# Kernel tuning notes

Measured on AMD Instinct MI355X. Metric: run time of the kernel, lower is better.

The kernel has to match this reference:

```python
import jax, jax.numpy as jnp
import numpy as np

N_EMBD = 1024
N_HEAD = 16

def setup_inputs() -> dict:
    key = jax.random.key(0)
    ks = jax.random.split(key, 5)
    x = jax.random.normal(ks[0], (4, 2048, N_EMBD), dtype=jnp.float32)
    # torch Linear default init ~ U(-1/sqrt(fan_in), 1/sqrt(fan_in)); use scaled normals
    s = 1.0 / np.sqrt(N_EMBD)
    W_attn = jax.random.normal(ks[1], (N_EMBD, 3 * N_EMBD), dtype=jnp.float32) * s
    b_attn = jax.random.normal(ks[2], (3 * N_EMBD,), dtype=jnp.float32) * s
    W_proj = jax.random.normal(ks[3], (N_EMBD, N_EMBD), dtype=jnp.float32) * s
    b_proj = jax.random.normal(ks[4], (N_EMBD,), dtype=jnp.float32) * s
    return {"x": x, "W_attn": W_attn, "b_attn": b_attn, "W_proj": W_proj, "b_proj": b_proj}

def reference(x, W_attn, b_attn, W_proj, b_proj) -> jnp.ndarray:
    B, T, C = x.shape
    H = N_HEAD
    D = C // H  # head dim
    qkv = x @ W_attn + b_attn  # [B,T,3C]
    q, k, v = jnp.split(qkv, 3, axis=-1)
    # [B,T,C] -> [B,H,T,D]
    q = q.reshape(B, T, H, D).transpose(0, 2, 1, 3)
    k = k.reshape(B, T, H, D).transpose(0, 2, 1, 3)
    v = v.reshape(B, T, H, D).transpose(0, 2, 1, 3)
    scale = 1.0 / jnp.sqrt(jnp.float32(D))
    att = jnp.einsum('bhqd,bhkd->bhqk', q, k) * scale  # [B,H,T,T]
    causal = jnp.tril(jnp.ones((T, T), dtype=bool))
    att = jnp.where(causal[None, None, :, :], att, -jnp.inf)
    att = jax.nn.softmax(att, axis=-1)
    y = jnp.einsum('bhqk,bhkd->bhqd', att, v)  # [B,H,T,D]
    y = y.transpose(0, 2, 1, 3).reshape(B, T, C)
    return y @ W_proj + b_proj
```

## Files before the change

### kernel.cpp

```cpp
#include <hip/hip_runtime.h>
#include <stdint.h>


typedef __attribute__((ext_vector_type(8))) short short8;
typedef __attribute__((ext_vector_type(4))) float floatx4;

#define AS1C(p) ((const __attribute__((address_space(1))) void*)(p))
#define AS3(p)  ((__attribute__((address_space(3))) void*)(p))

__device__ __forceinline__ unsigned short f2bf(float f) {
  unsigned int u = __builtin_bit_cast(unsigned int, f);
  u = (u + 0x7fffu + ((u >> 16) & 1u)) >> 16;
  return (unsigned short)u;
}
__device__ __forceinline__ unsigned short f2bf_trunc(float f) {
  return (unsigned short)(__builtin_bit_cast(unsigned int, f) >> 16);
}

__global__ void k_cvt(const float* __restrict__ in, unsigned short* __restrict__ out, int n4) {
  int i = blockIdx.x * blockDim.x + threadIdx.x;
  if (i < n4) {
    float4 v = ((const float4*)in)[i];
    ushort4 o;
    o.x = f2bf(v.x); o.y = f2bf(v.y); o.z = f2bf(v.z); o.w = f2bf(v.w);
    ((ushort4*)out)[i] = o;
  }
}

__global__ void k_tw(const float* __restrict__ in, unsigned short* __restrict__ out, int K, int N) {
  __shared__ float t[32][33];
  int n0 = blockIdx.x * 32, k0 = blockIdx.y * 32;
  int tx = threadIdx.x, ty = threadIdx.y;
#pragma unroll
  for (int i = 0; i < 4; i++)
    t[ty + 8 * i][tx] = in[(size_t)(k0 + ty + 8 * i) * N + n0 + tx];
  __syncthreads();
#pragma unroll
  for (int i = 0; i < 4; i++)
    out[(size_t)(n0 + ty + 8 * i) * K + k0 + tx] = f2bf(t[tx][ty + 8 * i]);
}

__global__ void k_tv(const unsigned short* __restrict__ qkv, unsigned short* __restrict__ vt) {
  __shared__ unsigned short t[32][33];
  int t0 = blockIdx.x * 32;
  int d0 = blockIdx.y * 32;
  int bh = blockIdx.z;
  int b = bh >> 4, h = bh & 15;
  int tx = threadIdx.x, ty = threadIdx.y;
#pragma unroll
  for (int i = 0; i < 4; i++)
    t[ty + 8 * i][tx] = qkv[(size_t)(b * 2048 + t0 + ty + 8 * i) * 3072 + 2048 + h * 64 + d0 + tx];
  __syncthreads();
#pragma unroll
  for (int i = 0; i < 4; i++)
    vt[(size_t)(bh * 64 + d0 + ty + 8 * i) * 2048 + t0 + tx] = t[tx][ty + 8 * i];
}

template <int OUT_F32>
__global__ __launch_bounds__(256)
void k_gemm(const unsigned short* __restrict__ A,
            const unsigned short* __restrict__ Bt,
            const float* __restrict__ bias,
            void* __restrict__ Cout, int M, int N, int K) {
  __shared__ unsigned short lA[128 * 64];
  __shared__ unsigned short lB[128 * 64];
  int tid = threadIdx.x;
  int lane = tid & 63, wv = tid >> 6;
  int lc = lane & 15, quad = lane >> 4;
  int m0 = blockIdx.y * 128, n0 = blockIdx.x * 128;
  int wm = (wv >> 1) * 64, wn = (wv & 1) * 64;
  int sw = lc & 7;

  floatx4 acc[4][4];
#pragma unroll
  for (int i = 0; i < 4; i++)
#pragma unroll
    for (int j = 0; j < 4; j++) acc[i][j] = (floatx4){0.f, 0.f, 0.f, 0.f};

  int srow = tid >> 3;
  int scol = (((tid & 7) ^ (srow & 7))) * 8;
  const unsigned short* gA = A + (size_t)(m0 + srow) * K + scol;
  const unsigned short* gB = Bt + (size_t)(n0 + srow) * K + scol;

  for (int k0 = 0; k0 < K; k0 += 64) {
#pragma unroll
    for (int c = 0; c < 4; c++) {
      __builtin_amdgcn_global_load_lds(AS1C(gA + (size_t)(32 * c) * K + k0),
                                       AS3(lA + (32 * c + 8 * wv) * 64), 16, 0, 0);
      __builtin_amdgcn_global_load_lds(AS1C(gB + (size_t)(32 * c) * K + k0),
                                       AS3(lB + (32 * c + 8 * wv) * 64), 16, 0, 0);
    }
    __syncthreads();
#pragma unroll
    for (int s = 0; s < 2; s++) {
      short8 af[4], bfr[4];
#pragma unroll
      for (int i = 0; i < 4; i++)
        af[i] = *(const short8*)(lA + (wm + i * 16 + lc) * 64 + (((s * 4 + quad) ^ sw) * 8));
#pragma unroll
      for (int j = 0; j < 4; j++)
        bfr[j] = *(const short8*)(lB + (wn + j * 16 + lc) * 64 + (((s * 4 + quad) ^ sw) * 8));
#pragma unroll
      for (int i = 0; i < 4; i++)
#pragma unroll
        for (int j = 0; j < 4; j++)
          acc[i][j] = __builtin_amdgcn_mfma_f32_16x16x32_bf16(af[i], bfr[j], acc[i][j], 0, 0, 0);
    }
    __syncthreads();
  }

  float bv[4];
#pragma unroll
  for (int j = 0; j < 4; j++) bv[j] = bias[n0 + wn + j * 16 + lc];
#pragma unroll
  for (int i = 0; i < 4; i++) {
#pragma unroll
    for (int j = 0; j < 4; j++) {
#pragma unroll
      for (int r = 0; r < 4; r++) {
        size_t idx = (size_t)(m0 + wm + i * 16 + quad * 4 + r) * N + (n0 + wn + j * 16 + lc);
        float v = acc[i][j][r] + bv[j];
        if (OUT_F32) ((float*)Cout)[idx] = v;
        else         ((unsigned short*)Cout)[idx] = f2bf(v);
      }
    }
  }
}

#define LP_STRIDE 68
__global__ __launch_bounds__(256, 4)
void k_flash(const unsigned short* __restrict__ qkv,
             const unsigned short* __restrict__ vt,
             unsigned short* __restrict__ y) {
  __shared__ unsigned short lK[64 * 64];
  __shared__ unsigned short lVT[64 * 64];
  __shared__ unsigned short lP[4][2][16 * LP_STRIDE];
  int tid = threadIdx.x, lane = tid & 63, wv = tid >> 6;
  int lc = lane & 15, quad = lane >> 4;
  int sw = lc & 7;
  int j  = blockIdx.x;
  int bh = blockIdx.y;
  int b = bh >> 4, h = bh & 15;
  int qtA = j, qtB = 31 - j;
  int qrA = qtA * 64 + wv * 16;
  int qrB = qtB * 64 + wv * 16;

  short8 qfA[2], qfB[2];
  {
    const unsigned short* qp = qkv + (size_t)(b * 2048 + qrA + lc) * 3072 + h * 64 + quad * 8;
    qfA[0] = *(const short8*)qp;
    qfA[1] = *(const short8*)(qp + 32);
  }
  {
    const unsigned short* qp = qkv + (size_t)(b * 2048 + qrB + lc) * 3072 + h * 64 + quad * 8;
    qfB[0] = *(const short8*)qp;
    qfB[1] = *(const short8*)(qp + 32);
  }

  float rsA[4] = {0.f, 0.f, 0.f, 0.f}, rsB[4] = {0.f, 0.f, 0.f, 0.f};
  floatx4 oA[4], oB[4];
#pragma unroll
  for (int dt = 0; dt < 4; dt++) {
    oA[dt] = (floatx4){0.f, 0.f, 0.f, 0.f};
    oB[dt] = (floatx4){0.f, 0.f, 0.f, 0.f};
  }

  int srow = tid >> 3;
  int scol = ((tid & 7) ^ (srow & 7)) * 8;
  const unsigned short* gK = qkv + (size_t)(b * 2048 + srow) * 3072 + 1024 + h * 64 + scol;
  const unsigned short* gV = vt + (size_t)(bh * 64 + srow) * 2048 + scol;

  const float SC2 = 0.18033688011f;
  int nt = qtB + 1;

  for (int kv = 0; kv < nt; kv++) {
    int kv0 = kv * 64;
#pragma unroll
    for (int c = 0; c < 2; c++) {
      __builtin_amdgcn_global_load_lds(AS1C(gK + (size_t)(kv0 + 32 * c) * 3072),
                                       AS3(lK + (32 * c + 8 * wv) * 64), 16, 0, 0);
      __builtin_amdgcn_global_load_lds(AS1C(gV + (size_t)(32 * c) * 2048 + kv0),
                                       AS3(lVT + (32 * c + 8 * wv) * 64), 16, 0, 0);
    }
    __syncthreads();

    bool withA = (kv <= qtA);

    floatx4 sB[4], sA[4];
#pragma unroll
    for (int n = 0; n < 4; n++) {
      short8 kf0 = *(const short8*)(lK + (n * 16 + lc) * 64 + ((quad ^ sw) * 8));
      short8 kf1 = *(const short8*)(lK + (n * 16 + lc) * 64 + (((4 + quad) ^ sw) * 8));
      floatx4 t = (floatx4){0.f, 0.f, 0.f, 0.f};
      t = __builtin_amdgcn_mfma_f32_16x16x32_bf16(qfB[0], kf0, t, 0, 0, 0);
      t = __builtin_amdgcn_mfma_f32_16x16x32_bf16(qfB[1], kf1, t, 0, 0, 0);
      sB[n] = t;
      if (withA) {
        floatx4 u = (floatx4){0.f, 0.f, 0.f, 0.f};
        u = __builtin_amdgcn_mfma_f32_16x16x32_bf16(qfA[0], kf0, u, 0, 0, 0);
        u = __builtin_amdgcn_mfma_f32_16x16x32_bf16(qfA[1], kf1, u, 0, 0, 0);
        sA[n] = u;
      }
    }

    {
      bool diag = (kv == qtB);
#pragma unroll
      for (int n = 0; n < 4; n++)
#pragma unroll
        for (int r = 0; r < 4; r++) {
          float arg = sB[n][r] * SC2;
          if (diag && (kv0 + n * 16 + lc > qrB + quad * 4 + r)) arg = -__builtin_inff();
          float p = __builtin_amdgcn_exp2f(arg);
          rsB[r] += p;
          lP[wv][0][(quad * 4 + r) * LP_STRIDE + n * 16 + lc] = f2bf_trunc(p);
        }
    }
    if (withA) {
      bool diag = (kv == qtA);
#pragma unroll
      for (int n = 0; n < 4; n++)
#pragma unroll
        for (int r = 0; r < 4; r++) {
          float arg = sA[n][r] * SC2;
          if (diag && (kv0 + n * 16 + lc > qrA + quad * 4 + r)) arg = -__builtin_inff();
          float p = __builtin_amdgcn_exp2f(arg);
          rsA[r] += p;
          lP[wv][1][(quad * 4 + r) * LP_STRIDE + n * 16 + lc] = f2bf_trunc(p);
        }
    }

#pragma unroll
    for (int s2 = 0; s2 < 2; s2++) {
      short8 pfB = *(const short8*)(&lP[wv][0][0] + lc * LP_STRIDE + s2 * 32 + quad * 8);
      short8 pfA;
      if (withA) pfA = *(const short8*)(&lP[wv][1][0] + lc * LP_STRIDE + s2 * 32 + quad * 8);
#pragma unroll
      for (int dt = 0; dt < 4; dt++) {
        short8 vf = *(const short8*)(lVT + (dt * 16 + lc) * 64 + (((s2 * 4 + quad) ^ sw) * 8));
        oB[dt] = __builtin_amdgcn_mfma_f32_16x16x32_bf16(pfB, vf, oB[dt], 0, 0, 0);
        if (withA) oA[dt] = __builtin_amdgcn_mfma_f32_16x16x32_bf16(pfA, vf, oA[dt], 0, 0, 0);
      }
    }
    __syncthreads();
  }

#pragma unroll
  for (int off = 1; off < 16; off <<= 1)
#pragma unroll
    for (int r = 0; r < 4; r++) {
      rsA[r] += __shfl_xor(rsA[r], off);
      rsB[r] += __shfl_xor(rsB[r], off);
    }
#pragma unroll
  for (int r = 0; r < 4; r++) {
    float invA = 1.0f / rsA[r];
    float invB = 1.0f / rsB[r];
#pragma unroll
    for (int dt = 0; dt < 4; dt++) {
      size_t ia = (size_t)(b * 2048 + qrA + quad * 4 + r) * 1024 + h * 64 + dt * 16 + lc;
      size_t ib = (size_t)(b * 2048 + qrB + quad * 4 + r) * 1024 + h * 64 + dt * 16 + lc;
      y[ia] = f2bf(oA[dt][r] * invA);
      y[ib] = f2bf(oB[dt][r] * invB);
    }
  }
}

extern "C" void kernel_launch(void* const* d_in, const int* in_sizes, int n_in,
                              void* d_out, int out_size, void* d_ws, size_t ws_size,
                              hipStream_t stream) {
  const float* x      = (const float*)d_in[0];
  const float* W_attn = (const float*)d_in[1];
  const float* b_attn = (const float*)d_in[2];
  const float* W_proj = (const float*)d_in[3];
  const float* b_proj = (const float*)d_in[4];

  char* ws = (char*)d_ws;
  unsigned short* xb     = (unsigned short*)ws;
  unsigned short* wattnT = (unsigned short*)(ws + 16777216);
  unsigned short* wprojT = (unsigned short*)(ws + 23068672);
  unsigned short* qkv    = (unsigned short*)(ws + 25165824);
  unsigned short* vt     = (unsigned short*)(ws + 75497472);
  unsigned short* y      = xb;

  k_cvt<<<8192, 256, 0, stream>>>(x, xb, 8388608 / 4);
  k_tw<<<dim3(96, 32), dim3(32, 8), 0, stream>>>(W_attn, wattnT, 1024, 3072);
  k_tw<<<dim3(32, 32), dim3(32, 8), 0, stream>>>(W_proj, wprojT, 1024, 1024);
  k_gemm<0><<<dim3(24, 64), 256, 0, stream>>>(xb, wattnT, b_attn, qkv, 8192, 3072, 1024);
  k_tv<<<dim3(64, 2, 64), dim3(32, 8), 0, stream>>>(qkv, vt);
  k_flash<<<dim3(16, 64), 256, 0, stream>>>(qkv, vt, y);
  k_gemm<1><<<dim3(8, 64), 256, 0, stream>>>(y, wprojT, b_proj, d_out, 8192, 1024, 1024);
}
```

Before: 271.0 us.

## Double-buffer K tiles, fold softmax scale into QKV GEMM, share P buffer

Adds a second LDS buffer for K so the next tile's K load is issued while the current tile is computed, and waits on only part of the vector-memory counter before the PV MFMAs. Removes the per-score scale multiply by folding the softmax scale into the Q columns in the QKV GEMM epilogue. Processes the B and A query tiles sequentially through one shared per-wave P buffer to cut LDS use. The hand-coded waitcnt immediate and the reuse of one P buffer add ordering risk. Folding the scale before the bf16 rounding of Q slightly changes numerics.

Measured after the change: 286.0 us. 5.6% more time.

```diff
diff --git a/kernel.cpp b/kernel.cpp
--- a/kernel.cpp
+++ b/kernel.cpp
@@ -7,6 +7,8 @@
 
 #define AS1C(p) ((const __attribute__((address_space(1))) void*)(p))
 #define AS3(p)  ((__attribute__((address_space(3))) void*)(p))
+
+#define SC2F 0.18033688011f
 
 __device__ __forceinline__ unsigned short f2bf(float f) {
   unsigned int u = __builtin_bit_cast(unsigned int, f);
@@ -116,10 +118,11 @@
   for (int i = 0; i < 4; i++) {
 #pragma unroll
     for (int j = 0; j < 4; j++) {
+      float sc = (!OUT_F32 && (n0 + wn + j * 16) < 1024) ? SC2F : 1.0f;
 #pragma unroll
       for (int r = 0; r < 4; r++) {
         size_t idx = (size_t)(m0 + wm + i * 16 + quad * 4 + r) * N + (n0 + wn + j * 16 + lc);
-        float v = acc[i][j][r] + bv[j];
+        float v = (acc[i][j][r] + bv[j]) * sc;
         if (OUT_F32) ((float*)Cout)[idx] = v;
         else         ((unsigned short*)Cout)[idx] = f2bf(v);
       }
@@ -132,9 +135,9 @@
 void k_flash(const unsigned short* __restrict__ qkv,
              const unsigned short* __restrict__ vt,
              unsigned short* __restrict__ y) {
-  __shared__ unsigned short lK[64 * 64];
+  __shared__ unsigned short lK[2][64 * 64];
   __shared__ unsigned short lVT[64 * 64];
-  __shared__ unsigned short lP[4][2][16 * LP_STRIDE];
+  __shared__ unsigned short lP[4][16 * LP_STRIDE];
   int tid = threadIdx.x, lane = tid & 63, wv = tid >> 6;
   int lc = lane & 15, quad = lane >> 4;
   int sw = lc & 7;
@@ -170,27 +173,35 @@
   const unsigned short* gK = qkv + (size_t)(b * 2048 + srow) * 3072 + 1024 + h * 64 + scol;
   const unsigned short* gV = vt + (size_t)(bh * 64 + srow) * 2048 + scol;
 
-  const float SC2 = 0.18033688011f;
   int nt = qtB + 1;
+
+#pragma unroll
+  for (int c = 0; c < 2; c++)
+    __builtin_amdgcn_global_load_lds(AS1C(gK + (size_t)(32 * c) * 3072),
+                                     AS3(lK[0] + (32 * c + 8 * wv) * 64), 16, 0, 0);
 
   for (int kv = 0; kv < nt; kv++) {
     int kv0 = kv * 64;
-#pragma unroll
-    for (int c = 0; c < 2; c++) {
-      __builtin_amdgcn_global_load_lds(AS1C(gK + (size_t)(kv0 + 32 * c) * 3072),
-                                       AS3(lK + (32 * c + 8 * wv) * 64), 16, 0, 0);
+    __syncthreads();
+
+#pragma unroll
+    for (int c = 0; c < 2; c++)
       __builtin_amdgcn_global_load_lds(AS1C(gV + (size_t)(32 * c) * 2048 + kv0),
                                        AS3(lVT + (32 * c + 8 * wv) * 64), 16, 0, 0);
-    }
-    __syncthreads();
-
+    int kp = (kv + 1 < nt) ? kv + 1 : kv;
+#pragma unroll
+    for (int c = 0; c < 2; c++)
+      __builtin_amdgcn_global_load_lds(AS1C(gK + (size_t)(kp * 64 + 32 * c) * 3072),
+                                       AS3(lK[(kv + 1) & 1] + (32 * c + 8 * wv) * 64), 16, 0, 0);
+
+    const unsigned short* kb = lK[kv & 1];
     bool withA = (kv <= qtA);
 
     floatx4 sB[4], sA[4];
 #pragma unroll
     for (int n = 0; n < 4; n++) {
-      short8 kf0 = *(const short8*)(lK + (n * 16 + lc) * 64 + ((quad ^ sw) * 8));
-      short8 kf1 = *(const short8*)(lK + (n * 16 + lc) * 64 + (((4 + quad) ^ sw) * 8));
+      short8 kf0 = *(const short8*)(kb + (n * 16 + lc) * 64 + ((quad ^ sw) * 8));
+      short8 kf1 = *(const short8*)(kb + (n * 16 + lc) * 64 + (((4 + quad) ^ sw) * 8));
       floatx4 t = (floatx4){0.f, 0.f, 0.f, 0.f};
       t = __builtin_amdgcn_mfma_f32_16x16x32_bf16(qfB[0], kf0, t, 0, 0, 0);
       t = __builtin_amdgcn_mfma_f32_16x16x32_bf16(qfB[1], kf1, t, 0, 0, 0);
@@ -209,40 +220,48 @@
       for (int n = 0; n < 4; n++)
 #pragma unroll
         for (int r = 0; r < 4; r++) {
-          float arg = sB[n][r] * SC2;
+          float arg = sB[n][r];
           if (diag && (kv0 + n * 16 + lc > qrB + quad * 4 + r)) arg = -__builtin_inff();
           float p = __builtin_amdgcn_exp2f(arg);
           rsB[r] += p;
-          lP[wv][0][(quad * 4 + r) * LP_STRIDE + n * 16 + lc] = f2bf_trunc(p);
+          lP[wv][(quad * 4 + r) * LP_STRIDE + n * 16 + lc] = f2bf_trunc(p);
         }
     }
+
+    __builtin_amdgcn_s_waitcnt(0x0F72);
+
+#pragma unroll
+    for (int s2 = 0; s2 < 2; s2++) {
+      short8 pfB = *(const short8*)(&lP[wv][0] + lc * LP_STRIDE + s2 * 32 + quad * 8);
+#pragma unroll
+      for (int dt = 0; dt < 4; dt++) {
+        short8 vf = *(const short8*)(lVT + (dt * 16 + lc) * 64 + (((s2 * 4 + quad) ^ sw) * 8));
+        oB[dt] = __builtin_amdgcn_mfma_f32_16x16x32_bf16(pfB, vf, oB[dt], 0, 0, 0);
+      }
+    }
+
     if (withA) {
       bool diag = (kv == qtA);
 #pragma unroll
       for (int n = 0; n < 4; n++)
 #pragma unroll
         for (int r = 0; r < 4; r++) {
-          float arg = sA[n][r] * SC2;
+          float arg = sA[n][r];
           if (diag && (kv0 + n * 16 + lc > qrA + quad * 4 + r)) arg = -__builtin_inff();
           float p = __builtin_amdgcn_exp2f(arg);
           rsA[r] += p;
-          lP[wv][1][(quad * 4 + r) * LP_STRIDE + n * 16 + lc] = f2bf_trunc(p);
+          lP[wv][(quad * 4 + r) * LP_STRIDE + n * 16 + lc] = f2bf_trunc(p);
         }
-    }
-
-#pragma unroll
-    for (int s2 = 0; s2 < 2; s2++) {
-      short8 pfB = *(const short8*)(&lP[wv][0][0] + lc * LP_STRIDE + s2 * 32 + quad * 8);
-      short8 pfA;
-      if (withA) pfA = *(const short8*)(&lP[wv][1][0] + lc * LP_STRIDE + s2 * 32 + quad * 8);
-#pragma unroll
-      for (int dt = 0; dt < 4; dt++) {
-        short8 vf = *(const short8*)(lVT + (dt * 16 + lc) * 64 + (((s2 * 4 + quad) ^ sw) * 8));
-        oB[dt] = __builtin_amdgcn_mfma_f32_16x16x32_bf16(pfB, vf, oB[dt], 0, 0, 0);
-        if (withA) oA[dt] = __builtin_amdgcn_mfma_f32_16x16x32_bf16(pfA, vf, oA[dt], 0, 0, 0);
+#pragma unroll
+      for (int s2 = 0; s2 < 2; s2++) {
+        short8 pfA = *(const short8*)(&lP[wv][0] + lc * LP_STRIDE + s2 * 32 + quad * 8);
+#pragma unroll
+        for (int dt = 0; dt < 4; dt++) {
+          short8 vf = *(const short8*)(lVT + (dt * 16 + lc) * 64 + (((s2 * 4 + quad) ^ sw) * 8));
+          oA[dt] = __builtin_amdgcn_mfma_f32_16x16x32_bf16(pfA, vf, oA[dt], 0, 0, 0);
+        }
       }
     }
-    __syncthreads();
   }
 
 #pragma unroll
```

## Remap blocks for XCD-local L2 reuse and fold softmax scale into Q

Applied to the files above, without the earlier changes.

Both GEMMs and the flash-attention kernel now launch a 1D grid and remap the block index so consecutive blocks on the same XCD share row tiles or the same batch-head. This is meant to improve L2 locality on the multi-XCD MI355X. Separately, the attention scale (log2e/sqrt(D)) is applied to the Q columns in the QKV GEMM epilogue, which removes a multiply per score in the flash inner loop. Pre-scaling Q before the bf16 rounding slightly changes the numerics.

After: 283.6 us. +4.6%, slower.

```diff
diff --git a/kernel.cpp b/kernel.cpp
--- a/kernel.cpp
+++ b/kernel.cpp
@@ -7,6 +7,8 @@
 
 #define AS1C(p) ((const __attribute__((address_space(1))) void*)(p))
 #define AS3(p)  ((__attribute__((address_space(3))) void*)(p))
+
+#define SC2F 0.18033688011f
 
 __device__ __forceinline__ unsigned short f2bf(float f) {
   unsigned int u = __builtin_bit_cast(unsigned int, f);
@@ -61,13 +63,17 @@
 void k_gemm(const unsigned short* __restrict__ A,
             const unsigned short* __restrict__ Bt,
             const float* __restrict__ bias,
-            void* __restrict__ Cout, int M, int N, int K) {
+            void* __restrict__ Cout, int M, int N, int K, int NX) {
   __shared__ unsigned short lA[128 * 64];
   __shared__ unsigned short lB[128 * 64];
+  int lin = blockIdx.x;
+  int xcd = lin & 7, idx = lin >> 3;
+  int bx = idx % NX;
+  int by = xcd + 8 * (idx / NX);
   int tid = threadIdx.x;
   int lane = tid & 63, wv = tid >> 6;
   int lc = lane & 15, quad = lane >> 4;
-  int m0 = blockIdx.y * 128, n0 = blockIdx.x * 128;
+  int m0 = by * 128, n0 = bx * 128;
   int wm = (wv >> 1) * 64, wn = (wv & 1) * 64;
   int sw = lc & 7;
 
@@ -116,12 +122,13 @@
   for (int i = 0; i < 4; i++) {
 #pragma unroll
     for (int j = 0; j < 4; j++) {
+      float sc = (!OUT_F32 && (n0 + wn + j * 16) < 1024) ? SC2F : 1.0f;
 #pragma unroll
       for (int r = 0; r < 4; r++) {
-        size_t idx = (size_t)(m0 + wm + i * 16 + quad * 4 + r) * N + (n0 + wn + j * 16 + lc);
-        float v = acc[i][j][r] + bv[j];
-        if (OUT_F32) ((float*)Cout)[idx] = v;
-        else         ((unsigned short*)Cout)[idx] = f2bf(v);
+        size_t idx2 = (size_t)(m0 + wm + i * 16 + quad * 4 + r) * N + (n0 + wn + j * 16 + lc);
+        float v = (acc[i][j][r] + bv[j]) * sc;
+        if (OUT_F32) ((float*)Cout)[idx2] = v;
+        else         ((unsigned short*)Cout)[idx2] = f2bf(v);
       }
     }
   }
@@ -138,8 +145,10 @@
   int tid = threadIdx.x, lane = tid & 63, wv = tid >> 6;
   int lc = lane & 15, quad = lane >> 4;
   int sw = lc & 7;
-  int j  = blockIdx.x;
-  int bh = blockIdx.y;
+  int lin = blockIdx.x;
+  int xcd = lin & 7, idx = lin >> 3;
+  int j   = idx & 15;
+  int bh  = xcd + 8 * (idx >> 4);
   int b = bh >> 4, h = bh & 15;
   int qtA = j, qtB = 31 - j;
   int qrA = qtA * 64 + wv * 16;
@@ -170,7 +179,6 @@
   const unsigned short* gK = qkv + (size_t)(b * 2048 + srow) * 3072 + 1024 + h * 64 + scol;
   const unsigned short* gV = vt + (size_t)(bh * 64 + srow) * 2048 + scol;
 
-  const float SC2 = 0.18033688011f;
   int nt = qtB + 1;
 
   for (int kv = 0; kv < nt; kv++) {
@@ -209,7 +217,7 @@
       for (int n = 0; n < 4; n++)
 #pragma unroll
         for (int r = 0; r < 4; r++) {
-          float arg = sB[n][r] * SC2;
+          float arg = sB[n][r];
           if (diag && (kv0 + n * 16 + lc > qrB + quad * 4 + r)) arg = -__builtin_inff();
           float p = __builtin_amdgcn_exp2f(arg);
           rsB[r] += p;
@@ -222,7 +230,7 @@
       for (int n = 0; n < 4; n++)
 #pragma unroll
         for (int r = 0; r < 4; r++) {
-          float arg = sA[n][r] * SC2;
+          float arg = sA[n][r];
           if (diag && (kv0 + n * 16 + lc > qrA + quad * 4 + r)) arg = -__builtin_inff();
           float p = __builtin_amdgcn_exp2f(arg);
           rsA[r] += p;
@@ -286,8 +294,8 @@
   k_cvt<<<8192, 256, 0, stream>>>(x, xb, 8388608 / 4);
   k_tw<<<dim3(96, 32), dim3(32, 8), 0, stream>>>(W_attn, wattnT, 1024, 3072);
   k_tw<<<dim3(32, 32), dim3(32, 8), 0, stream>>>(W_proj, wprojT, 1024, 1024);
-  k_gemm<0><<<dim3(24, 64), 256, 0, stream>>>(xb, wattnT, b_attn, qkv, 8192, 3072, 1024);
+  k_gemm<0><<<24 * 64, 256, 0, stream>>>(xb, wattnT, b_attn, qkv, 8192, 3072, 1024, 24);
   k_tv<<<dim3(64, 2, 64), dim3(32, 8), 0, stream>>>(qkv, vt);
-  k_flash<<<dim3(16, 64), 256, 0, stream>>>(qkv, vt, y);
-  k_gemm<1><<<dim3(8, 64), 256, 0, stream>>>(y, wprojT, b_proj, d_out, 8192, 1024, 1024);
-}
+  k_flash<<<1024, 256, 0, stream>>>(qkv, vt, y);
+  k_gemm<1><<<8 * 64, 256, 0, stream>>>(y, wprojT, b_proj, d_out, 8192, 1024, 1024, 8);
+}
```
